# Performance work log

Measured on AMD Instinct MI355X. Metric: run time of the kernel, lower is better.

## Reference

```python
import jax, jax.numpy as jnp
import numpy as np

# NF4 codebook (bitsandbytes nf4 data type, 16 levels)
NF4_TABLE = np.array([
    -1.0, -0.6961928009986877, -0.5250730514526367, -0.39491748809814453,
    -0.28444138169288635, -0.18477343022823334, -0.09105003625154495, 0.0,
    0.07958029955625534, 0.16093020141124725, 0.24611230194568634,
    0.33791524171829224, 0.44070982933044434, 0.5626170039176941,
    0.7229568362236023, 1.0], dtype=np.float32)

BLOCKSIZE = 64
SCALING = 32.0 / 16.0  # lora_alpha / r


def setup_inputs() -> dict:
    key = jax.random.key(0)
    k1, k2, k3, k4, k5 = jax.random.split(key, 5)
    tokens, in_f, out_f, r = 256, 4096, 11008, 16
    x = jax.random.normal(k1, (tokens, in_f), dtype=jnp.float32)
    q_codes = jax.random.randint(k2, (out_f, in_f), 0, 16, dtype=jnp.int32)
    absmax = jax.random.uniform(k3, (out_f, in_f // BLOCKSIZE), dtype=jnp.float32)
    lora_A = jax.random.normal(k4, (r, in_f), dtype=jnp.float32) * (1.0 / np.sqrt(in_f))
    lora_B = jax.random.normal(k5, (out_f, r), dtype=jnp.float32) * 0.02
    return {"x": x, "q_codes": q_codes, "absmax": absmax,
            "lora_A": lora_A, "lora_B": lora_B}


def reference(x, q_codes, absmax, lora_A, lora_B):
    out_f, in_f = q_codes.shape
    nf4 = jnp.asarray(NF4_TABLE, dtype=x.dtype)
    # Dequantize: codebook lookup, then per-block absmax scale.
    W = nf4[q_codes].reshape(out_f, in_f // BLOCKSIZE, BLOCKSIZE)
    W = (W * absmax[:, :, None]).reshape(out_f, in_f)  # [out_f, in_f]
    # Base 4-bit linear (no bias in bnb Linear4bit default here).
    base = x @ W.T  # [tokens, out_f]
    # LoRA path: dropout p=0 is identity in eval; scaling = alpha/r.
    lora = (x @ lora_A.T) @ lora_B.T  # [tokens, r] -> [tokens, out_f]
    return base + lora * jnp.asarray(SCALING, dtype=x.dtype)
```

## Files before the change

### kernel.cpp

```cpp
#include <hip/hip_runtime.h>

typedef unsigned int uint;
typedef unsigned short ushort;

typedef __attribute__((ext_vector_type(8))) short bf16x8;
typedef __attribute__((ext_vector_type(4))) float f32x4;

#define TOK 256
#define OUTF 11008
#define INF 4096
#define BM 256
#define BN 32
#define BK 64
#define NKT 64

__device__ __constant__ float NF4_TBL[16] = {
    -1.0f, -0.6961928009986877f, -0.5250730514526367f, -0.39491748809814453f,
    -0.28444138169288635f, -0.18477343022823334f, -0.09105003625154495f, 0.0f,
    0.07958029955625534f, 0.16093020141124725f, 0.24611230194568634f,
    0.33791524171829224f, 0.44070982933044434f, 0.5626170039176941f,
    0.7229568362236023f, 1.0f};

__device__ __forceinline__ ushort f2bf(float f) {
  return (ushort)((__float_as_uint(f) + 0x8000u) >> 16);
}

__device__ __forceinline__ void async_cp16(const void* g, void* l) {
  __builtin_amdgcn_global_load_lds(
      (const __attribute__((address_space(1))) uint*)g,
      (__attribute__((address_space(3))) uint*)l, 16, 0, 0);
}

__device__ __forceinline__ uint dq2(int ca, int cb, float amax, int tbits) {
  float fa = __int_as_float(__builtin_amdgcn_ds_bpermute(ca << 2, tbits)) * amax;
  float fb = __int_as_float(__builtin_amdgcn_ds_bpermute(cb << 2, tbits)) * amax;
  uint ua = (__float_as_uint(fa) + 0x8000u) >> 16;
  uint ub = (__float_as_uint(fb) + 0x8000u) & 0xffff0000u;
  return ua | ub;
}

__global__ void prep_kernel(const float* __restrict__ x, const float* __restrict__ lB,
                            ushort* __restrict__ xbf, ushort* __restrict__ lBbf) {
  const int stride = gridDim.x * blockDim.x;
  for (int idx = blockIdx.x * blockDim.x + threadIdx.x; idx < TOK * INF; idx += stride)
    xbf[idx] = f2bf(x[idx]);
  for (int idx = blockIdx.x * blockDim.x + threadIdx.x; idx < OUTF * 64; idx += stride) {
    int n = idx >> 6, j = idx & 63;
    lBbf[idx] = (j < 16) ? f2bf(lB[n * 16 + j]) : (ushort)0;
  }
}

__global__ void xa_kernel(const float* __restrict__ x, const float* __restrict__ lA,
                          ushort* __restrict__ xa2) {
  const int m = blockIdx.x;
  const int t = threadIdx.x;
  float acc[16];
#pragma unroll
  for (int j = 0; j < 16; ++j) acc[j] = 0.f;
  for (int kk = 0; kk < 16; ++kk) {
    int k = kk * 256 + t;
    float xv = x[m * INF + k];
#pragma unroll
    for (int j = 0; j < 16; ++j) acc[j] += xv * lA[j * INF + k];
  }
#pragma unroll
  for (int j = 0; j < 16; ++j)
#pragma unroll
    for (int s = 32; s > 0; s >>= 1) acc[j] += __shfl_xor(acc[j], s, 64);
  __shared__ float red[4][16];
  const int w = t >> 6, l = t & 63;
  if (l == 0) {
#pragma unroll
    for (int j = 0; j < 16; ++j) red[w][j] = acc[j];
  }
  __syncthreads();
  if (t < 64) {
    ushort v = 0;
    if (t < 16) {
      float s = red[0][t] + red[1][t] + red[2][t] + red[3][t];
      v = f2bf(2.0f * s);
    }
    xa2[m * 64 + t] = v;
  }
}

__global__ __launch_bounds__(256, 2)
void gemm_kernel(const int* __restrict__ qc, const float* __restrict__ am,
                 const ushort* __restrict__ xbf, const ushort* __restrict__ lBbf,
                 const ushort* __restrict__ xa2, float* __restrict__ out) {
  __shared__ ushort Abuf[BM * BK];
  __shared__ ushort Bbuf[BN * BK];

  const int tid = threadIdx.x;
  const int w = tid >> 6;
  const int l = tid & 63;
  const int n0 = blockIdx.x * BN;

  const int tbits = __float_as_int(NF4_TBL[l & 15]);

  const int arow = w * 8 + (l >> 3);
  const int acol = ((l & 7) ^ (l >> 3)) << 3;

  const int brow = tid >> 3;
  const int bq = tid & 7;

  int aoff[2][4], boff[2][2];
#pragma unroll
  for (int ks = 0; ks < 2; ++ks) {
    const int cc = ks * 4 + (l >> 4);
#pragma unroll
    for (int mt = 0; mt < 4; ++mt) {
      int row = w * 64 + mt * 16 + (l & 15);
      aoff[ks][mt] = row * 64 + ((cc ^ (l & 7)) << 3);
    }
#pragma unroll
    for (int nt = 0; nt < 2; ++nt) {
      int row = nt * 16 + (l & 15);
      boff[ks][nt] = row * 64 + ((cc ^ (l & 7)) << 3);
    }
  }

  f32x4 acc[4][2];
#pragma unroll
  for (int mt = 0; mt < 4; ++mt)
#pragma unroll
    for (int nt = 0; nt < 2; ++nt) acc[mt][nt] = (f32x4){0.f, 0.f, 0.f, 0.f};

  for (int kt = 0; kt <= NKT; ++kt) {
    if (kt < NKT) {
#pragma unroll
      for (int i = 0; i < 8; ++i) {
        const ushort* g = xbf + (size_t)(i * 32 + arow) * INF + kt * BK + acol;
        async_cp16(g, &Abuf[(i * 256 + w * 64) * 8]);
      }
      const int* qrow = qc + (size_t)(n0 + brow) * INF + kt * BK + bq * 8;
      int4 c0 = ((const int4*)qrow)[0];
      int4 c1 = ((const int4*)qrow)[1];
      float amax = am[(n0 + brow) * 64 + kt];
      uint4 d;
      d.x = dq2(c0.x, c0.y, amax, tbits);
      d.y = dq2(c0.z, c0.w, amax, tbits);
      d.z = dq2(c1.x, c1.y, amax, tbits);
      d.w = dq2(c1.z, c1.w, amax, tbits);
      *(uint4*)&Bbuf[(brow * 8 + (bq ^ (brow & 7))) * 8] = d;
    } else {
#pragma unroll
      for (int i = 0; i < 8; ++i) {
        const ushort* g = xa2 + (i * 32 + arow) * 64 + acol;
        async_cp16(g, &Abuf[(i * 256 + w * 64) * 8]);
      }
      const ushort* g = lBbf + (size_t)(n0 + arow) * 64 + acol;
      async_cp16(g, &Bbuf[(w * 64) * 8]);
    }
    __syncthreads();
#pragma unroll
    for (int ks = 0; ks < 2; ++ks) {
      bf16x8 a[4], b[2];
#pragma unroll
      for (int mt = 0; mt < 4; ++mt) a[mt] = *(const bf16x8*)&Abuf[aoff[ks][mt]];
#pragma unroll
      for (int nt = 0; nt < 2; ++nt) b[nt] = *(const bf16x8*)&Bbuf[boff[ks][nt]];
#pragma unroll
      for (int mt = 0; mt < 4; ++mt)
#pragma unroll
        for (int nt = 0; nt < 2; ++nt)
          acc[mt][nt] = __builtin_amdgcn_mfma_f32_16x16x32_bf16(a[mt], b[nt], acc[mt][nt], 0, 0, 0);
    }
    __syncthreads();
  }

#pragma unroll
  for (int mt = 0; mt < 4; ++mt) {
#pragma unroll
    for (int nt = 0; nt < 2; ++nt) {
      int col = n0 + nt * 16 + (l & 15);
#pragma unroll
      for (int r = 0; r < 4; ++r) {
        int row = w * 64 + mt * 16 + (l >> 4) * 4 + r;
        out[(size_t)row * OUTF + col] = acc[mt][nt][r];
      }
    }
  }
}

extern "C" void kernel_launch(void* const* d_in, const int* in_sizes, int n_in,
                              void* d_out, int out_size, void* d_ws, size_t ws_size,
                              hipStream_t stream) {
  const float* x = (const float*)d_in[0];
  const int* qc = (const int*)d_in[1];
  const float* am = (const float*)d_in[2];
  const float* lA = (const float*)d_in[3];
  const float* lB = (const float*)d_in[4];
  float* out = (float*)d_out;

  ushort* xbf = (ushort*)d_ws;
  ushort* lBbf = xbf + (size_t)TOK * INF;
  ushort* xa2 = lBbf + (size_t)OUTF * 64;

  prep_kernel<<<1024, 256, 0, stream>>>(x, lB, xbf, lBbf);
  xa_kernel<<<TOK, 256, 0, stream>>>(x, lA, xa2);
  gemm_kernel<<<OUTF / BN, 256, 0, stream>>>(qc, am, xbf, lBbf, xa2, out);
}
```

Before: 332.7 us.

## Add split-K GEMM with partial buffers, register prefetch, and vectorized prep kernels

Splits the K dimension of the dequant GEMM across up to 4 blocks per N-tile, chosen by available workspace. Each split writes fp32 partials and a separate reduce kernel sums them. The change prefetches the next tile's NF4 codes and absmax into registers, raises the occupancy hint, and vectorizes the bf16 conversion and x@A^T kernels with float4 and 1024-thread blocks. The aim is to fill the GPU better than 344 blocks can. The cost is extra partial-sum traffic and a reduction pass.

```diff
diff --git a/kernel.cpp b/kernel.cpp
--- a/kernel.cpp
+++ b/kernel.cpp
@@ -13,6 +13,7 @@
 #define BN 32
 #define BK 64
 #define NKT 64
+#define NTILES 344
 
 __device__ __constant__ float NF4_TBL[16] = {
     -1.0f, -0.6961928009986877f, -0.5250730514526367f, -0.39491748809814453f,
@@ -39,35 +40,45 @@
   return ua | ub;
 }
 
-__global__ void prep_kernel(const float* __restrict__ x, const float* __restrict__ lB,
-                            ushort* __restrict__ xbf, ushort* __restrict__ lBbf) {
+__global__ void prep_kernel(const float4* __restrict__ x4, const float4* __restrict__ lB4,
+                            ushort4* __restrict__ xbf4, ushort4* __restrict__ lBbf4) {
   const int stride = gridDim.x * blockDim.x;
-  for (int idx = blockIdx.x * blockDim.x + threadIdx.x; idx < TOK * INF; idx += stride)
-    xbf[idx] = f2bf(x[idx]);
-  for (int idx = blockIdx.x * blockDim.x + threadIdx.x; idx < OUTF * 64; idx += stride) {
-    int n = idx >> 6, j = idx & 63;
-    lBbf[idx] = (j < 16) ? f2bf(lB[n * 16 + j]) : (ushort)0;
-  }
-}
-
-__global__ void xa_kernel(const float* __restrict__ x, const float* __restrict__ lA,
-                          ushort* __restrict__ xa2) {
+  for (int idx = blockIdx.x * blockDim.x + threadIdx.x; idx < TOK * INF / 4; idx += stride) {
+    float4 v = x4[idx];
+    ushort4 o;
+    o.x = f2bf(v.x); o.y = f2bf(v.y); o.z = f2bf(v.z); o.w = f2bf(v.w);
+    xbf4[idx] = o;
+  }
+  for (int idx = blockIdx.x * blockDim.x + threadIdx.x; idx < OUTF * 16; idx += stride) {
+    int n = idx >> 4, jq = idx & 15;
+    ushort4 o = {0, 0, 0, 0};
+    if (jq < 4) {
+      float4 v = lB4[n * 4 + jq];
+      o.x = f2bf(v.x); o.y = f2bf(v.y); o.z = f2bf(v.z); o.w = f2bf(v.w);
+    }
+    lBbf4[idx] = o;
+  }
+}
+
+__global__ __launch_bounds__(1024)
+void xa_kernel(const float* __restrict__ x, const float* __restrict__ lA,
+               ushort* __restrict__ xa2) {
   const int m = blockIdx.x;
   const int t = threadIdx.x;
+  const float4* x4 = (const float4*)(x + (size_t)m * INF);
+  const float4* lA4 = (const float4*)lA;
+  float4 xv = x4[t];
   float acc[16];
 #pragma unroll
-  for (int j = 0; j < 16; ++j) acc[j] = 0.f;
-  for (int kk = 0; kk < 16; ++kk) {
-    int k = kk * 256 + t;
-    float xv = x[m * INF + k];
-#pragma unroll
-    for (int j = 0; j < 16; ++j) acc[j] += xv * lA[j * INF + k];
+  for (int j = 0; j < 16; ++j) {
+    float4 a = lA4[j * (INF / 4) + t];
+    acc[j] = xv.x * a.x + xv.y * a.y + xv.z * a.z + xv.w * a.w;
   }
 #pragma unroll
   for (int j = 0; j < 16; ++j)
 #pragma unroll
     for (int s = 32; s > 0; s >>= 1) acc[j] += __shfl_xor(acc[j], s, 64);
-  __shared__ float red[4][16];
+  __shared__ float red[16][16];
   const int w = t >> 6, l = t & 63;
   if (l == 0) {
 #pragma unroll
@@ -77,24 +88,31 @@
   if (t < 64) {
     ushort v = 0;
     if (t < 16) {
-      float s = red[0][t] + red[1][t] + red[2][t] + red[3][t];
+      float s = 0.f;
+#pragma unroll
+      for (int w2 = 0; w2 < 16; ++w2) s += red[w2][t];
       v = f2bf(2.0f * s);
     }
     xa2[m * 64 + t] = v;
   }
 }
 
-__global__ __launch_bounds__(256, 2)
+__global__ __launch_bounds__(256, 4)
 void gemm_kernel(const int* __restrict__ qc, const float* __restrict__ am,
                  const ushort* __restrict__ xbf, const ushort* __restrict__ lBbf,
-                 const ushort* __restrict__ xa2, float* __restrict__ out) {
+                 const ushort* __restrict__ xa2, float* __restrict__ dest,
+                 int kt_per) {
   __shared__ ushort Abuf[BM * BK];
   __shared__ ushort Bbuf[BN * BK];
 
   const int tid = threadIdx.x;
   const int w = tid >> 6;
   const int l = tid & 63;
-  const int n0 = blockIdx.x * BN;
+  const int split = blockIdx.x / NTILES;
+  const int ntile = blockIdx.x - split * NTILES;
+  const int n0 = ntile * BN;
+  const int k0t = split * kt_per;
+  const int ktEnd = k0t + kt_per;
 
   const int tbits = __float_as_int(NF4_TBL[l & 15]);
 
@@ -126,31 +144,28 @@
 #pragma unroll
     for (int nt = 0; nt < 2; ++nt) acc[mt][nt] = (f32x4){0.f, 0.f, 0.f, 0.f};
 
-  for (int kt = 0; kt <= NKT; ++kt) {
-    if (kt < NKT) {
-#pragma unroll
-      for (int i = 0; i < 8; ++i) {
-        const ushort* g = xbf + (size_t)(i * 32 + arow) * INF + kt * BK + acol;
-        async_cp16(g, &Abuf[(i * 256 + w * 64) * 8]);
-      }
-      const int* qrow = qc + (size_t)(n0 + brow) * INF + kt * BK + bq * 8;
-      int4 c0 = ((const int4*)qrow)[0];
-      int4 c1 = ((const int4*)qrow)[1];
-      float amax = am[(n0 + brow) * 64 + kt];
-      uint4 d;
-      d.x = dq2(c0.x, c0.y, amax, tbits);
-      d.y = dq2(c0.z, c0.w, amax, tbits);
-      d.z = dq2(c1.x, c1.y, amax, tbits);
-      d.w = dq2(c1.z, c1.w, amax, tbits);
-      *(uint4*)&Bbuf[(brow * 8 + (bq ^ (brow & 7))) * 8] = d;
-    } else {
-#pragma unroll
-      for (int i = 0; i < 8; ++i) {
-        const ushort* g = xa2 + (i * 32 + arow) * 64 + acol;
-        async_cp16(g, &Abuf[(i * 256 + w * 64) * 8]);
-      }
-      const ushort* g = lBbf + (size_t)(n0 + arow) * 64 + acol;
-      async_cp16(g, &Bbuf[(w * 64) * 8]);
+  const int* qbase = qc + (size_t)(n0 + brow) * INF + bq * 8;
+  const float* ambase = am + (size_t)(n0 + brow) * 64;
+  int4 c0 = ((const int4*)(qbase + (size_t)k0t * BK))[0];
+  int4 c1 = ((const int4*)(qbase + (size_t)k0t * BK))[1];
+  float amax = ambase[k0t];
+
+  for (int kt = k0t; kt < ktEnd; ++kt) {
+#pragma unroll
+    for (int i = 0; i < 8; ++i) {
+      const ushort* g = xbf + (size_t)(i * 32 + arow) * INF + kt * BK + acol;
+      async_cp16(g, &Abuf[(i * 256 + w * 64) * 8]);
+    }
+    uint4 d;
+    d.x = dq2(c0.x, c0.y, amax, tbits);
+    d.y = dq2(c0.z, c0.w, amax, tbits);
+    d.z = dq2(c1.x, c1.y, amax, tbits);
+    d.w = dq2(c1.z, c1.w, amax, tbits);
+    *(uint4*)&Bbuf[(brow * 8 + (bq ^ (brow & 7))) * 8] = d;
+    if (kt + 1 < ktEnd) {
+      c0 = ((const int4*)(qbase + (size_t)(kt + 1) * BK))[0];
+      c1 = ((const int4*)(qbase + (size_t)(kt + 1) * BK))[1];
+      amax = ambase[kt + 1];
     }
     __syncthreads();
 #pragma unroll
@@ -169,6 +184,32 @@
     __syncthreads();
   }
 
+  if (split == 0) {
+#pragma unroll
+    for (int i = 0; i < 8; ++i) {
+      const ushort* g = xa2 + (i * 32 + arow) * 64 + acol;
+      async_cp16(g, &Abuf[(i * 256 + w * 64) * 8]);
+    }
+    const ushort* g = lBbf + (size_t)(n0 + arow) * 64 + acol;
+    async_cp16(g, &Bbuf[(w * 64) * 8]);
+    __syncthreads();
+#pragma unroll
+    for (int ks = 0; ks < 2; ++ks) {
+      bf16x8 a[4], b[2];
+#pragma unroll
+      for (int mt = 0; mt < 4; ++mt) a[mt] = *(const bf16x8*)&Abuf[aoff[ks][mt]];
+#pragma unroll
+      for (int nt = 0; nt < 2; ++nt) b[nt] = *(const bf16x8*)&Bbuf[boff[ks][nt]];
+#pragma unroll
+      for (int mt = 0; mt < 4; ++mt)
+#pragma unroll
+        for (int nt = 0; nt < 2; ++nt)
+          acc[mt][nt] = __builtin_amdgcn_mfma_f32_16x16x32_bf16(a[mt], b[nt], acc[mt][nt], 0, 0, 0);
+    }
+    __syncthreads();
+  }
+
+  float* dst = dest + (size_t)split * TOK * OUTF;
 #pragma unroll
   for (int mt = 0; mt < 4; ++mt) {
 #pragma unroll
@@ -177,9 +218,23 @@
 #pragma unroll
       for (int r = 0; r < 4; ++r) {
         int row = w * 64 + mt * 16 + (l >> 4) * 4 + r;
-        out[(size_t)row * OUTF + col] = acc[mt][nt][r];
+        dst[(size_t)row * OUTF + col] = acc[mt][nt][r];
       }
     }
+  }
+}
+
+__global__ void reduce_kernel(const float4* __restrict__ part, float4* __restrict__ out,
+                              int ks) {
+  const int QN = TOK * OUTF / 4;
+  int i = blockIdx.x * blockDim.x + threadIdx.x;
+  if (i < QN) {
+    float4 s = part[i];
+    for (int s2 = 1; s2 < ks; ++s2) {
+      float4 p = part[(size_t)s2 * QN + i];
+      s.x += p.x; s.y += p.y; s.z += p.z; s.w += p.w;
+    }
+    out[i] = s;
   }
 }
 
@@ -193,11 +248,26 @@
   const float* lB = (const float*)d_in[4];
   float* out = (float*)d_out;
 
+  const size_t off_lB = (size_t)TOK * INF * 2;
+  const size_t off_xa2 = off_lB + (size_t)OUTF * 64 * 2;
+  const size_t off_part = off_xa2 + (size_t)TOK * 64 * 2;
+  const size_t part_bytes = (size_t)TOK * OUTF * 4;
+
   ushort* xbf = (ushort*)d_ws;
-  ushort* lBbf = xbf + (size_t)TOK * INF;
-  ushort* xa2 = lBbf + (size_t)OUTF * 64;
-
-  prep_kernel<<<1024, 256, 0, stream>>>(x, lB, xbf, lBbf);
-  xa_kernel<<<TOK, 256, 0, stream>>>(x, lA, xa2);
-  gemm_kernel<<<OUTF / BN, 256, 0, stream>>>(qc, am, xbf, lBbf, xa2, out);
-}
+  ushort* lBbf = (ushort*)((char*)d_ws + off_lB);
+  ushort* xa2 = (ushort*)((char*)d_ws + off_xa2);
+  float* part = (float*)((char*)d_ws + off_part);
+
+  int ks = 1;
+  if (ws_size >= off_part + 4 * part_bytes) ks = 4;
+  else if (ws_size >= off_part + 2 * part_bytes) ks = 2;
+  float* dest = (ks == 1) ? out : part;
+
+  prep_kernel<<<1024, 256, 0, stream>>>((const float4*)x, (const float4*)lB,
+                                        (ushort4*)xbf, (ushort4*)lBbf);
+  xa_kernel<<<TOK, 1024, 0, stream>>>(x, lA, xa2);
+  gemm_kernel<<<NTILES * ks, 256, 0, stream>>>(qc, am, xbf, lBbf, xa2, dest, NKT / ks);
+  if (ks > 1)
+    reduce_kernel<<<(TOK * OUTF / 4 + 255) / 256, 256, 0, stream>>>((const float4*)part,
+                                                                    (float4*)out, ks);
+}
```

Result: faster. 318.2 us (-4.3%).
